# Kernel tuning notes

Measured on AMD Instinct MI355X. Metric: run time of the kernel, lower is better.

The kernel has to match this reference:

```python
import jax, jax.numpy as jnp
import numpy as np

B, T, D, U = 32, 2048, 1024, 1024

def setup_inputs() -> dict:
    key = jax.random.key(0)
    ks = jax.random.split(key, 8)
    s = 0.02
    return {
        "query": jax.random.normal(ks[0], (B, D), dtype=jnp.float32),
        "values": jax.random.normal(ks[1], (B, T, D), dtype=jnp.float32),
        "W1": jax.random.normal(ks[2], (D, U), dtype=jnp.float32) * s,
        "b1": jnp.zeros((U,), dtype=jnp.float32),
        "W2": jax.random.normal(ks[3], (D, U), dtype=jnp.float32) * s,
        "b2": jnp.zeros((U,), dtype=jnp.float32),
        "V": jax.random.normal(ks[4], (U, 1), dtype=jnp.float32) * s,
        "bv": jnp.zeros((1,), dtype=jnp.float32),
    }

def reference(query, values, W1, b1, W2, b2, V, bv):
    # query: [B, D] -> [B, 1, U] via W2; values: [B, T, D] -> [B, T, U] via W1
    q_proj = query @ W2 + b2                     # [B, U]
    v_proj = jnp.einsum('btd,du->btu', values, W1) + b1   # [B, T, U]
    # score: Dense(1) on tanh(sum) -> [B, T, 1]
    score = jnp.tanh(v_proj + q_proj[:, None, :]) @ V + bv  # [B, T, 1]
    attention_weights = jax.nn.softmax(score, axis=1)        # softmax over time
    context_vector = jnp.sum(attention_weights * values, axis=1)  # [B, D]
    return context_vector, attention_weights
```

## Files before the change

### kernel.cpp

```cpp
#include <hip/hip_runtime.h>
#include <hip/hip_bf16.h>
#include <stdint.h>

#define WS_W1F   0
#define WS_QP2   2097152
#define WS_ESC   (WS_QP2 + 131072)
#define WS_PCTX  (WS_ESC + 262144)
#define WS_PDEN  (WS_PCTX + 4194304)
#define WS_NEED  (WS_PDEN + 4096)

typedef __attribute__((ext_vector_type(8))) short bf16x8;
typedef __attribute__((ext_vector_type(4))) float f32x4;

__device__ inline uint16_t f2b(float f) {
    __hip_bfloat16 h = __float2bfloat16(f);
    return *reinterpret_cast<uint16_t*>(&h);
}

__global__ __launch_bounds__(256) void k_prep(const float* __restrict__ W1,
                                              const float* __restrict__ query,
                                              const float* __restrict__ W2,
                                              const float* __restrict__ b1,
                                              const float* __restrict__ b2,
                                              __hip_bfloat16* __restrict__ W1f,
                                              float* __restrict__ qp2,
                                              float* __restrict__ zctx,
                                              float* __restrict__ zden) {
    __shared__ float qs[1024];
    int blk = blockIdx.x, tid = threadIdx.x;
    if (blk < 256) {
        int lane = tid & 63, fi = tid >> 6;
        int l15 = lane & 15, quad = lane >> 4;
        #pragma unroll
        for (int p = 0; p < 2; ++p) {
            int frag = blk * 8 + p * 4 + fi;
            int ut = frag >> 5, ks = frag & 31;
            union { uint16_t h[8]; int4 v; } pk;
            #pragma unroll
            for (int j = 0; j < 8; ++j) {
                float x = W1[(size_t)(ks * 32 + quad * 8 + j) * 1024 + ut * 16 + l15];
                pk.h[j] = f2b(x);
            }
            *(int4*)((char*)W1f + (size_t)frag * 1024 + lane * 16) = pk.v;
        }
    } else {
        int bq = blk - 256;
        int b = bq >> 2, qc = bq & 3;
        if (zctx != nullptr && qc == 0) {
            *(float4*)(zctx + b * 1024 + tid * 4) = make_float4(0.f, 0.f, 0.f, 0.f);
            if (b == 0 && tid < 32) zden[tid] = 0.f;
        }
        int u = qc * 256 + tid;
        const float* q = query + b * 1024;
        #pragma unroll
        for (int i = 0; i < 4; ++i) qs[i * 256 + tid] = q[i * 256 + tid];
        __syncthreads();
        float a = b1[u] + b2[u];
        #pragma unroll 8
        for (int d = 0; d < 1024; ++d)
            a += qs[d] * W2[(size_t)d * 1024 + u];
        qp2[b * 1024 + u] = a;
    }
}

__global__ __launch_bounds__(512, 1) void k_score(
        const float* __restrict__ values, const __hip_bfloat16* __restrict__ W1f,
        const float* __restrict__ qp2, const float* __restrict__ V,
        float* __restrict__ escore, float* __restrict__ pctx,
        float* __restrict__ pden, float* __restrict__ ctxa) {
    extern __shared__ char smem[];
    uint16_t* Al = (uint16_t*)smem;
    float* red = (float*)(smem + 131072);

    const int tid = threadIdx.x;
    const int lane = tid & 63, w = tid >> 6;
    const int quad = lane >> 4, l15 = lane & 15;
    const int b = blockIdx.x >> 5, trow0 = (blockIdx.x & 31) << 6;

    const float* Ag = values + (size_t)(b * 2048 + trow0) * 1024;
    #pragma unroll
    for (int i = 0; i < 16; ++i) {
        int id = i * 512 + tid;
        int row = id >> 7, c = id & 127;
        const float* src = Ag + (size_t)row * 1024 + c * 8;
        float4 v0 = *(const float4*)src;
        float4 v1 = *(const float4*)(src + 4);
        union { uint16_t h[8]; int4 v; } pk;
        pk.h[0]=f2b(v0.x); pk.h[1]=f2b(v0.y); pk.h[2]=f2b(v0.z); pk.h[3]=f2b(v0.w);
        pk.h[4]=f2b(v1.x); pk.h[5]=f2b(v1.y); pk.h[6]=f2b(v1.z); pk.h[7]=f2b(v1.w);
        int pos = (c & 112) | ((c & 15) ^ (row & 15));
        *(int4*)(Al + (size_t)row * 1024 + pos * 8) = pk.v;
    }
    __syncthreads();

    const char* Bbase = (const char*)W1f + (size_t)(w * 8) * 32768 + lane * 16;

    f32x4 acc[4][8];
    #pragma unroll
    for (int rt = 0; rt < 4; ++rt)
        #pragma unroll
        for (int ct = 0; ct < 8; ++ct) acc[rt][ct] = (f32x4){0.f, 0.f, 0.f, 0.f};

    bf16x8 af[2][4], bfr[2][8];
    {
        int pos = (quad & 15) ^ l15;
        #pragma unroll
        for (int rt = 0; rt < 4; ++rt)
            af[0][rt] = *(bf16x8*)(Al + (rt * 16 + l15) * 1024 + pos * 8);
        #pragma unroll
        for (int ct = 0; ct < 8; ++ct)
            bfr[0][ct] = *(const bf16x8*)(Bbase + (size_t)(ct * 32) * 1024);
    }

    #pragma unroll 2
    for (int ks = 0; ks < 32; ++ks) {
        int cur = ks & 1, nxt = cur ^ 1;
        if (ks < 31) {
            int cb = (ks + 1) * 4 + quad;
            int pos = (cb & 112) | ((cb & 15) ^ l15);
            #pragma unroll
            for (int rt = 0; rt < 4; ++rt)
                af[nxt][rt] = *(bf16x8*)(Al + (rt * 16 + l15) * 1024 + pos * 8);
            #pragma unroll
            for (int ct = 0; ct < 8; ++ct)
                bfr[nxt][ct] = *(const bf16x8*)(Bbase + (size_t)(ct * 32 + ks + 1) * 1024);
        }
        #pragma unroll
        for (int rt = 0; rt < 4; ++rt)
            #pragma unroll
            for (int ct = 0; ct < 8; ++ct)
                acc[rt][ct] = __builtin_amdgcn_mfma_f32_16x16x32_bf16(
                    af[cur][rt], bfr[cur][ct], acc[rt][ct], 0, 0, 0);
    }

    float srow[4][4];
    #pragma unroll
    for (int rt = 0; rt < 4; ++rt)
        #pragma unroll
        for (int r = 0; r < 4; ++r) srow[rt][r] = 0.f;
    #pragma unroll
    for (int ct = 0; ct < 8; ++ct) {
        int u = w * 128 + ct * 16 + l15;
        float qv = qp2[b * 1024 + u];
        float vv = V[u];
        #pragma unroll
        for (int rt = 0; rt < 4; ++rt)
            #pragma unroll
            for (int r = 0; r < 4; ++r) {
                float x = acc[rt][ct][r] + qv;
                float e = __expf(2.f * x);
                float t = 1.f - 2.f * __builtin_amdgcn_rcpf(1.f + e);
                srow[rt][r] += t * vv;
            }
    }

    #pragma unroll
    for (int rt = 0; rt < 4; ++rt)
        #pragma unroll
        for (int r = 0; r < 4; ++r) {
            float s = srow[rt][r];
            s += __shfl_xor(s, 1, 64);
            s += __shfl_xor(s, 2, 64);
            s += __shfl_xor(s, 4, 64);
            s += __shfl_xor(s, 8, 64);
            srow[rt][r] = s;
        }
    if (l15 == 0) {
        #pragma unroll
        for (int rt = 0; rt < 4; ++rt)
            #pragma unroll
            for (int r = 0; r < 4; ++r)
                red[w * 64 + rt * 16 + quad * 4 + r] = srow[rt][r];
    }
    __syncthreads();

    float* wl = (float*)smem;
    if (tid < 64) {
        float s = 0.f;
        #pragma unroll
        for (int k = 0; k < 8; ++k) s += red[k * 64 + tid];
        float e = __expf(s);
        escore[b * 2048 + trow0 + tid] = e;
        wl[tid] = e;
        float dsum = e;
        #pragma unroll
        for (int off = 32; off; off >>= 1) dsum += __shfl_xor(dsum, off, 64);
        if (tid == 0) {
            if (pctx != nullptr) pden[blockIdx.x] = dsum;
            else                 atomicAdd(&pden[b], dsum);
        }
    }
    __syncthreads();

    {
        const float* Vg = values + (size_t)(b * 2048 + trow0) * 1024 + tid * 2;
        float ax = 0.f, ay = 0.f;
        #pragma unroll 8
        for (int t = 0; t < 64; ++t) {
            float wv = wl[t];
            float2 v = *(const float2*)(Vg + (size_t)t * 1024);
            ax += wv * v.x; ay += wv * v.y;
        }
        if (pctx != nullptr) {
            *(float2*)(pctx + (size_t)blockIdx.x * 1024 + tid * 2) = make_float2(ax, ay);
        } else {
            float* o = ctxa + b * 1024 + tid * 2;
            atomicAdd(o + 0, ax);
            atomicAdd(o + 1, ay);
        }
    }
}

__global__ __launch_bounds__(256) void k_final(const float* __restrict__ pctx,
                                               const float* __restrict__ pden,
                                               const float* __restrict__ escore,
                                               float* __restrict__ out) {
    __shared__ float sinv;
    int b = blockIdx.x, tid = threadIdx.x;
    if (tid == 0) {
        float dsum = 0.f;
        if (pctx != nullptr) {
            #pragma unroll
            for (int t = 0; t < 32; ++t) dsum += pden[b * 32 + t];
        } else {
            dsum = pden[b];
        }
        sinv = 1.f / dsum;
    }
    __syncthreads();
    float inv = sinv;

    int d = tid * 4;
    if (pctx != nullptr) {
        float4 a = {0.f, 0.f, 0.f, 0.f};
        #pragma unroll 8
        for (int t = 0; t < 32; ++t) {
            float4 p = *(const float4*)(pctx + (size_t)(b * 32 + t) * 1024 + d);
            a.x += p.x; a.y += p.y; a.z += p.z; a.w += p.w;
        }
        a.x *= inv; a.y *= inv; a.z *= inv; a.w *= inv;
        *(float4*)(out + b * 1024 + d) = a;
    } else {
        float4 a = *(const float4*)(out + b * 1024 + d);
        a.x *= inv; a.y *= inv; a.z *= inv; a.w *= inv;
        *(float4*)(out + b * 1024 + d) = a;
    }

    #pragma unroll
    for (int i = 0; i < 8; ++i) {
        int t = i * 256 + tid;
        out[32768 + b * 2048 + t] = escore[b * 2048 + t] * inv;
    }
}

extern "C" void kernel_launch(void* const* d_in, const int* in_sizes, int n_in,
                              void* d_out, int out_size, void* d_ws, size_t ws_size,
                              hipStream_t stream) {
    const float* query  = (const float*)d_in[0];
    const float* values = (const float*)d_in[1];
    const float* W1 = (const float*)d_in[2];
    const float* b1 = (const float*)d_in[3];
    const float* W2 = (const float*)d_in[4];
    const float* b2 = (const float*)d_in[5];
    const float* V  = (const float*)d_in[6];

    char* ws = (char*)d_ws;
    __hip_bfloat16* W1f = (__hip_bfloat16*)(ws + WS_W1F);
    float* qp2 = (float*)(ws + WS_QP2);
    float* out = (float*)d_out;

    const bool big = ws_size >= (size_t)WS_NEED;
    float* escore = big ? (float*)(ws + WS_ESC)  : out + 32768;
    float* pctx   = big ? (float*)(ws + WS_PCTX) : nullptr;
    float* pden   = big ? (float*)(ws + WS_PDEN) : (float*)(ws + WS_ESC);
    float* zctx   = big ? nullptr : out;
    float* zden   = big ? nullptr : pden;

    (void)hipFuncSetAttribute((const void*)k_score,
                              hipFuncAttributeMaxDynamicSharedMemorySize, 133120);

    k_prep<<<384, 256, 0, stream>>>(W1, query, W2, b1, b2, W1f, qp2, zctx, zden);
    k_score<<<1024, 512, 133120, stream>>>(values, W1f, qp2, V, escore, pctx, pden, out);
    k_final<<<32, 256, 0, stream>>>(pctx, pden, escore, out);
}
```

Measured before the change: 579.8 us.

## Stream A from global per k-step and stage W1 via global_load_lds

```diff
diff --git a/kernel.cpp b/kernel.cpp
--- a/kernel.cpp
+++ b/kernel.cpp
@@ -15,6 +15,12 @@
 __device__ inline uint16_t f2b(float f) {
     __hip_bfloat16 h = __float2bfloat16(f);
     return *reinterpret_cast<uint16_t*>(&h);
+}
+
+__device__ inline void gl_lds16(const void* g, void* l) {
+    __builtin_amdgcn_global_load_lds(
+        (const __attribute__((address_space(1))) uint32_t*)g,
+        (__attribute__((address_space(3))) uint32_t*)l, 16, 0, 0);
 }
 
 __global__ __launch_bounds__(256) void k_prep(const float* __restrict__ W1,
@@ -27,6 +33,7 @@
                                               float* __restrict__ zctx,
                                               float* __restrict__ zden) {
     __shared__ float qs[1024];
+    __shared__ float part[4][64];
     int blk = blockIdx.x, tid = threadIdx.x;
     if (blk < 256) {
         int lane = tid & 63, fi = tid >> 6;
@@ -45,31 +52,38 @@
         }
     } else {
         int bq = blk - 256;
-        int b = bq >> 2, qc = bq & 3;
-        if (zctx != nullptr && qc == 0) {
+        int b = bq >> 4, us = bq & 15, u0 = us * 64;
+        if (zctx != nullptr && us == 0) {
             *(float4*)(zctx + b * 1024 + tid * 4) = make_float4(0.f, 0.f, 0.f, 0.f);
             if (b == 0 && tid < 32) zden[tid] = 0.f;
         }
-        int u = qc * 256 + tid;
         const float* q = query + b * 1024;
         #pragma unroll
         for (int i = 0; i < 4; ++i) qs[i * 256 + tid] = q[i * 256 + tid];
         __syncthreads();
-        float a = b1[u] + b2[u];
+        int ul = tid & 63, g = tid >> 6;
+        float a = 0.f;
+        const float* w2p = W2 + (size_t)(g * 256) * 1024 + u0 + ul;
+        const float* qg = qs + g * 256;
         #pragma unroll 8
-        for (int d = 0; d < 1024; ++d)
-            a += qs[d] * W2[(size_t)d * 1024 + u];
-        qp2[b * 1024 + u] = a;
-    }
-}
-
-__global__ __launch_bounds__(512, 1) void k_score(
+        for (int d = 0; d < 256; ++d)
+            a += qg[d] * w2p[(size_t)d * 1024];
+        part[g][ul] = a;
+        __syncthreads();
+        if (tid < 64) {
+            float r = part[0][tid] + part[1][tid] + part[2][tid] + part[3][tid]
+                    + b1[u0 + tid] + b2[u0 + tid];
+            qp2[b * 1024 + u0 + tid] = r;
+        }
+    }
+}
+
+__global__ __launch_bounds__(512, 2) void k_score(
         const float* __restrict__ values, const __hip_bfloat16* __restrict__ W1f,
         const float* __restrict__ qp2, const float* __restrict__ V,
         float* __restrict__ escore, float* __restrict__ pctx,
         float* __restrict__ pden, float* __restrict__ ctxa) {
     extern __shared__ char smem[];
-    uint16_t* Al = (uint16_t*)smem;
     float* red = (float*)(smem + 131072);
 
     const int tid = threadIdx.x;
@@ -77,23 +91,9 @@
     const int quad = lane >> 4, l15 = lane & 15;
     const int b = blockIdx.x >> 5, trow0 = (blockIdx.x & 31) << 6;
 
-    const float* Ag = values + (size_t)(b * 2048 + trow0) * 1024;
-    #pragma unroll
-    for (int i = 0; i < 16; ++i) {
-        int id = i * 512 + tid;
-        int row = id >> 7, c = id & 127;
-        const float* src = Ag + (size_t)row * 1024 + c * 8;
-        float4 v0 = *(const float4*)src;
-        float4 v1 = *(const float4*)(src + 4);
-        union { uint16_t h[8]; int4 v; } pk;
-        pk.h[0]=f2b(v0.x); pk.h[1]=f2b(v0.y); pk.h[2]=f2b(v0.z); pk.h[3]=f2b(v0.w);
-        pk.h[4]=f2b(v1.x); pk.h[5]=f2b(v1.y); pk.h[6]=f2b(v1.z); pk.h[7]=f2b(v1.w);
-        int pos = (c & 112) | ((c & 15) ^ (row & 15));
-        *(int4*)(Al + (size_t)row * 1024 + pos * 8) = pk.v;
-    }
-    __syncthreads();
-
-    const char* Bbase = (const char*)W1f + (size_t)(w * 8) * 32768 + lane * 16;
+    const float* Ab = values + (size_t)(b * 2048 + trow0 + l15) * 1024 + quad * 8;
+    const char* Bsrc = (const char*)W1f + (size_t)(w * 8) * 32768 + lane * 16;
+    char* Bdst = smem + w * 8192;
 
     f32x4 acc[4][8];
     #pragma unroll
@@ -101,36 +101,56 @@
         #pragma unroll
         for (int ct = 0; ct < 8; ++ct) acc[rt][ct] = (f32x4){0.f, 0.f, 0.f, 0.f};
 
-    bf16x8 af[2][4], bfr[2][8];
-    {
-        int pos = (quad & 15) ^ l15;
-        #pragma unroll
-        for (int rt = 0; rt < 4; ++rt)
-            af[0][rt] = *(bf16x8*)(Al + (rt * 16 + l15) * 1024 + pos * 8);
-        #pragma unroll
-        for (int ct = 0; ct < 8; ++ct)
-            bfr[0][ct] = *(const bf16x8*)(Bbase + (size_t)(ct * 32) * 1024);
-    }
+    asm volatile("s_waitcnt vmcnt(0)" ::: "memory");
+
+    float4 raw[4][2];
+    #pragma unroll
+    for (int rt = 0; rt < 4; ++rt) {
+        const float* p = Ab + (size_t)rt * 16 * 1024;
+        raw[rt][0] = *(const float4*)p;
+        raw[rt][1] = *(const float4*)(p + 4);
+    }
+    #pragma unroll
+    for (int ct = 0; ct < 8; ++ct)
+        gl_lds16(Bsrc + (size_t)(ct * 32) * 1024, Bdst + ct * 1024);
 
     #pragma unroll 2
     for (int ks = 0; ks < 32; ++ks) {
-        int cur = ks & 1, nxt = cur ^ 1;
+        const int cur = ks & 1;
+        bf16x8 afb[4];
+        #pragma unroll
+        for (int rt = 0; rt < 4; ++rt) {
+            union { uint16_t h[8]; bf16x8 v; } pk;
+            pk.h[0] = f2b(raw[rt][0].x); pk.h[1] = f2b(raw[rt][0].y);
+            pk.h[2] = f2b(raw[rt][0].z); pk.h[3] = f2b(raw[rt][0].w);
+            pk.h[4] = f2b(raw[rt][1].x); pk.h[5] = f2b(raw[rt][1].y);
+            pk.h[6] = f2b(raw[rt][1].z); pk.h[7] = f2b(raw[rt][1].w);
+            afb[rt] = pk.v;
+        }
         if (ks < 31) {
-            int cb = (ks + 1) * 4 + quad;
-            int pos = (cb & 112) | ((cb & 15) ^ l15);
+            #pragma unroll
+            for (int rt = 0; rt < 4; ++rt) {
+                const float* p = Ab + (size_t)rt * 16 * 1024 + (ks + 1) * 32;
+                raw[rt][0] = *(const float4*)p;
+                raw[rt][1] = *(const float4*)(p + 4);
+            }
+            #pragma unroll
+            for (int ct = 0; ct < 8; ++ct)
+                gl_lds16(Bsrc + (size_t)(ct * 32 + ks + 1) * 1024,
+                         Bdst + (cur ^ 1) * 65536 + ct * 1024);
+            asm volatile("s_waitcnt vmcnt(16)" ::: "memory");
+        } else {
+            asm volatile("s_waitcnt vmcnt(0)" ::: "memory");
+        }
+        __builtin_amdgcn_sched_barrier(0);
+        #pragma unroll
+        for (int ct = 0; ct < 8; ++ct) {
+            bf16x8 bq = *(bf16x8*)(smem + cur * 65536 + w * 8192 + ct * 1024 + lane * 16);
             #pragma unroll
             for (int rt = 0; rt < 4; ++rt)
-                af[nxt][rt] = *(bf16x8*)(Al + (rt * 16 + l15) * 1024 + pos * 8);
-            #pragma unroll
-            for (int ct = 0; ct < 8; ++ct)
-                bfr[nxt][ct] = *(const bf16x8*)(Bbase + (size_t)(ct * 32 + ks + 1) * 1024);
-        }
-        #pragma unroll
-        for (int rt = 0; rt < 4; ++rt)
-            #pragma unroll
-            for (int ct = 0; ct < 8; ++ct)
                 acc[rt][ct] = __builtin_amdgcn_mfma_f32_16x16x32_bf16(
-                    af[cur][rt], bfr[cur][ct], acc[rt][ct], 0, 0, 0);
+                    afb[rt], bq, acc[rt][ct], 0, 0, 0);
+        }
     }
 
     float srow[4][4];
@@ -279,7 +299,7 @@
     (void)hipFuncSetAttribute((const void*)k_score,
                               hipFuncAttributeMaxDynamicSharedMemorySize, 133120);
 
-    k_prep<<<384, 256, 0, stream>>>(W1, query, W2, b1, b2, W1f, qp2, zctx, zden);
+    k_prep<<<768, 256, 0, stream>>>(W1, query, W2, b1, b2, W1f, qp2, zctx, zden);
     k_score<<<1024, 512, 133120, stream>>>(values, W1f, qp2, V, escore, pctx, pden, out);
     k_final<<<32, 256, 0, stream>>>(pctx, pden, escore, out);
 }
```

After: 666.7 us. 15.0% more time.
